# Kernel tuning notes

Measured on AMD Instinct MI355X. Metric: run time of the kernel, lower is better.

The kernel has to match this reference:

```python
import jax, jax.numpy as jnp
import numpy as np

B, M, IN, HID, A = 4096, 64, 3, 128, 64
D = 50.0                       # waveguide_bound
H_CONST = 5.0
PMAX = 10.0 ** (30 / 10 - 3)   # = 1.0 (30 dBm in Watts)
C_LIGHT = 3.0e8
FC = 6.0e9
DELTA_MIN = (C_LIGHT / FC) / 2.0  # 0.025
ALPHA = 0.2                    # LeakyReLU slope


def setup_inputs() -> dict:
    key = jax.random.key(0)
    ks = jax.random.split(key, 9)
    s = lambda k, sh: (jax.random.normal(k, sh, jnp.float32) * 0.1)
    return {
        "users": jax.random.normal(ks[0], (B, M, IN), jnp.float32),
        "W1": s(ks[1], (IN, HID)),    # GAT layer 1 projection (applied as h @ W)
        "a1": s(ks[2], (2 * HID,)),   # GAT layer 1 attention vector
        "W2": s(ks[3], (HID, HID)),   # GAT layer 2 projection
        "a2": s(ks[4], (2 * HID,)),
        "mw1": s(ks[5], (HID, 32)),   # MLP Linear(hidden, 32)
        "mb1": jnp.zeros((32,), jnp.float32),
        "mw2": s(ks[6], (32, 2 * A)), # MLP Linear(32, 2*num_antennas)
        "mb2": jnp.zeros((2 * A,), jnp.float32),
    }


def gat_layer(h, W, a):
    # Wh: [B, M, d]
    Wh = h @ W
    d = W.shape[1]
    # e[b,i,j] = leakyrelu( cat(Wh_i, Wh_j) . a ) = leakyrelu( Wh_i.a[:d] + Wh_j.a[d:] )
    si = Wh @ a[:d]          # [B, M]
    sj = Wh @ a[d:]          # [B, M]
    e = jax.nn.leaky_relu(si[:, :, None] + sj[:, None, :], ALPHA)  # [B, M, M]
    attn = jax.nn.softmax(e, axis=-1)  # softmax over neighbors j (dropout p=0 -> identity)
    h_prime = jnp.einsum('bij,bjd->bid', attn, Wh)
    return jax.nn.elu(h_prime)


def reference(users, W1, a1, W2, a2, mw1, mb1, mw2, mb2):
    h = gat_layer(users, W1, a1)
    h = gat_layer(h, W2, a2)
    pooled = jnp.max(h, axis=1)                      # [B, hidden]
    readout = jax.nn.relu(pooled @ mw1 + mb1) @ mw2 + mb2  # [B, 2A]
    raw_delta, raw_power = readout[:, :A], readout[:, A:]
    eps = 1e-6
    raw_delta = jax.nn.relu(raw_delta) + eps
    raw_power = jax.nn.relu(raw_power) + eps
    Bmax = 2.0 * D - (A - 1) * DELTA_MIN
    delta = Bmax * raw_delta / (jnp.sum(raw_delta, axis=1, keepdims=True) + eps)
    power = PMAX * raw_power / (jnp.sum(raw_power, axis=1, keepdims=True) + eps)
    return power, delta
```

## Files before the change

kernel.cpp:

```cpp
#include <hip/hip_runtime.h>

#define NBATCH 4096
#define OUT2 (NBATCH * 64)

typedef _Float16 f16;
typedef __attribute__((ext_vector_type(8))) _Float16 f16x8;
typedef __attribute__((ext_vector_type(4))) _Float16 f16x4;
typedef __attribute__((ext_vector_type(4))) float f32x4;

__device__ __forceinline__ float lrelu(float x) { return x > 0.0f ? x : 0.2f * x; }
__device__ __forceinline__ float elu1(float x)  { return x > 0.0f ? x : __expf(x) - 1.0f; }

__global__ void prep(const float* __restrict__ W2, const float* __restrict__ W1,
                     const float* __restrict__ a1, const float* __restrict__ a2,
                     f16* __restrict__ w2b, float* __restrict__ w2a, float* __restrict__ w1a) {
    const int flat = blockIdx.x * 256 + threadIdx.x;
    const int slot = flat >> 3, j = flat & 7;
    const int F2T = slot >> 8, kf = (slot >> 6) & 3, ln = slot & 63;
    const int lq = ln >> 4, lr = ln & 15;
    w2b[flat] = (f16)W2[(kf * 32 + lq * 8 + j) * 128 + F2T * 16 + lr];
    if (blockIdx.x == 0) {
        if (threadIdx.x < 128) {
            const int f1 = threadIdx.x;
            float si = 0.f, sj = 0.f;
            for (int f2 = 0; f2 < 128; ++f2) {
                const float w = W2[f1 * 128 + f2];
                si = fmaf(w, a2[f2], si);
                sj = fmaf(w, a2[128 + f2], sj);
            }
            w2a[f1] = si; w2a[128 + f1] = sj;
        } else if (threadIdx.x < 131) {
            const int c = threadIdx.x - 128;
            float si = 0.f, sj = 0.f;
            for (int f = 0; f < 128; ++f) {
                const float w = W1[c * 128 + f];
                si = fmaf(w, a1[f], si);
                sj = fmaf(w, a1[128 + f], sj);
            }
            w1a[c] = si; w1a[3 + c] = sj;
        }
    }
}

__global__ __launch_bounds__(64)
void gat_kernel(const float* __restrict__ users,
                const float* __restrict__ W1,
                const f16* __restrict__ w2b,
                const float* __restrict__ w1a,
                const float* __restrict__ w2a,
                const float* __restrict__ mw1,
                const float* __restrict__ mb1,
                const float* __restrict__ mw2,
                const float* __restrict__ mb2,
                float* __restrict__ out)
{
    const int b = blockIdx.x;
    const int lane = threadIdx.x;
    const int lr = lane & 15;
    const int lq = lane >> 4;

    __shared__ __align__(16) char smem[10752];
    f16*   sMain = (f16*)smem;
    f16*   sBn   = (f16*)(smem + 8192);
    float* sPool = (float*)(smem + 8192);
    float* sHid  = (float*)(smem + 8704);
    float* sSi   = (float*)(smem + 10240);
    float* sSj   = (float*)(smem + 10496);

    {
        const float* u = users + b * 192;
        const float x = u[lane * 3], y = u[lane * 3 + 1], z = u[lane * 3 + 2];
        sSi[lane] = fmaf(x, w1a[0], fmaf(y, w1a[1], z * w1a[2]));
        sSj[lane] = fmaf(x, w1a[3], fmaf(y, w1a[4], z * w1a[5]));
    }
    __syncthreads();
    float mj;
    {
        float v = sSj[lane];
        #pragma unroll
        for (int m = 1; m < 64; m <<= 1) v = fmaxf(v, __shfl_xor(v, m, 64));
        mj = v;
    }

    f16x8 hf[4][4];

    #pragma unroll
    for (int h = 0; h < 2; ++h) {
        f16x8 bw[4];
        #pragma unroll
        for (int ntl = 0; ntl < 4; ++ntl) {
            #pragma unroll
            for (int j = 0; j < 8; ++j) bw[ntl][j] = (f16)0.f;
            if (lq == 0) {
                #pragma unroll
                for (int j = 0; j < 3; ++j)
                    bw[ntl][j] = (f16)W1[j * 128 + h * 64 + ntl * 16 + lr];
            }
        }
        #pragma unroll
        for (int mt = 0; mt < 4; ++mt) {
            f16x8 af;
            #pragma unroll
            for (int j = 0; j < 8; ++j) af[j] = (f16)0.f;
            if (lq == 0) {
                const float* up = users + b * 192 + (mt * 16 + lr) * 3;
                af[0] = (f16)up[0]; af[1] = (f16)up[1]; af[2] = (f16)up[2];
            }
            #pragma unroll
            for (int ntl = 0; ntl < 4; ++ntl) {
                f32x4 acc = (f32x4){0.f, 0.f, 0.f, 0.f};
                acc = __builtin_amdgcn_mfma_f32_16x16x32_f16(af, bw[ntl], acc, 0, 0, 0);
                const int fl = ntl * 16 + lr;
                const int g = mt * 2 + (lq >> 1);
                const int base = fl * 64 + ((g ^ (fl & 7)) << 3) + ((lq & 1) * 4);
                f16x4 hv;
                #pragma unroll
                for (int r = 0; r < 4; ++r) hv[r] = (f16)acc[r];
                *(f16x4*)&sMain[base] = hv;
            }
        }
        __syncthreads();

        #pragma unroll
        for (int mt = 0; mt < 4; ++mt) {
            const float si = sSi[mt * 16 + lr];
            const float mi = lrelu(si + mj);
            f16x8 ap0, ap1;
            float lsum = 0.f;
            #pragma unroll
            for (int jj = 0; jj < 8; ++jj) {
                float p = __expf(lrelu(si + sSj[lq * 8 + jj]) - mi);
                f16 ph = (f16)p; lsum += (float)ph; ap0[jj] = ph;
                p = __expf(lrelu(si + sSj[32 + lq * 8 + jj]) - mi);
                ph = (f16)p; lsum += (float)ph; ap1[jj] = ph;
            }
            lsum += __shfl_xor(lsum, 16, 64);
            lsum += __shfl_xor(lsum, 32, 64);
            const float inv = 1.0f / lsum;
            float invr[4];
            #pragma unroll
            for (int r = 0; r < 4; ++r) invr[r] = __shfl(inv, lq * 4 + r, 64);

            f32x4 acc[4];
            #pragma unroll
            for (int ntl = 0; ntl < 4; ++ntl) {
                const int fl = ntl * 16 + lr;
                f16x8 b0 = *(const f16x8*)&sMain[fl * 64 + ((lq ^ (fl & 7)) << 3)];
                f16x8 b1 = *(const f16x8*)&sMain[fl * 64 + (((4 + lq) ^ (fl & 7)) << 3)];
                acc[ntl] = (f32x4){0.f, 0.f, 0.f, 0.f};
                acc[ntl] = __builtin_amdgcn_mfma_f32_16x16x32_f16(ap0, b0, acc[ntl], 0, 0, 0);
                acc[ntl] = __builtin_amdgcn_mfma_f32_16x16x32_f16(ap1, b1, acc[ntl], 0, 0, 0);
            }
            __syncthreads();
            #pragma unroll
            for (int ntl = 0; ntl < 4; ++ntl) {
                const int fl = ntl * 16 + lr;
                #pragma unroll
                for (int r = 0; r < 4; ++r) {
                    const int nl = lq * 4 + r;
                    const float v = elu1(acc[ntl][r] * invr[r]);
                    sBn[nl * 64 + (((fl >> 3) ^ (nl & 7)) << 3) + (fl & 7)] = (f16)v;
                }
            }
            __syncthreads();
            #pragma unroll
            for (int ksl = 0; ksl < 2; ++ksl)
                hf[mt][h * 2 + ksl] =
                    *(const f16x8*)&sBn[lr * 64 + (((ksl * 4 + lq) ^ (lr & 7)) << 3)];
        }
        __syncthreads();
    }

    {
        float s2i[4] = {0.f, 0.f, 0.f, 0.f}, s2j[4] = {0.f, 0.f, 0.f, 0.f};
        #pragma unroll
        for (int ks = 0; ks < 4; ++ks) {
            float wi[8], wj[8];
            *(float4*)&wi[0] = *(const float4*)&w2a[ks * 32 + lq * 8];
            *(float4*)&wi[4] = *(const float4*)&w2a[ks * 32 + lq * 8 + 4];
            *(float4*)&wj[0] = *(const float4*)&w2a[128 + ks * 32 + lq * 8];
            *(float4*)&wj[4] = *(const float4*)&w2a[128 + ks * 32 + lq * 8 + 4];
            #pragma unroll
            for (int mt = 0; mt < 4; ++mt) {
                #pragma unroll
                for (int jj = 0; jj < 8; ++jj) {
                    const float v = (float)hf[mt][ks][jj];
                    s2i[mt] = fmaf(v, wi[jj], s2i[mt]);
                    s2j[mt] = fmaf(v, wj[jj], s2j[mt]);
                }
            }
        }
        #pragma unroll
        for (int mt = 0; mt < 4; ++mt) {
            s2i[mt] += __shfl_xor(s2i[mt], 16, 64);
            s2i[mt] += __shfl_xor(s2i[mt], 32, 64);
            s2j[mt] += __shfl_xor(s2j[mt], 16, 64);
            s2j[mt] += __shfl_xor(s2j[mt], 32, 64);
        }
        if (lq == 0) {
            #pragma unroll
            for (int mt = 0; mt < 4; ++mt) {
                sSi[mt * 16 + lr] = s2i[mt];
                sSj[mt * 16 + lr] = s2j[mt];
            }
        }
        __syncthreads();
    }
    float mj2;
    {
        float v = sSj[lane];
        #pragma unroll
        for (int m = 1; m < 64; m <<= 1) v = fmaxf(v, __shfl_xor(v, m, 64));
        mj2 = v;
    }

    #pragma unroll
    for (int h = 0; h < 2; ++h) {
        #pragma unroll
        for (int f2t = 0; f2t < 4; ++f2t) {
            f16x8 bw2[4];
            #pragma unroll
            for (int kf = 0; kf < 4; ++kf)
                bw2[kf] = *(const f16x8*)(w2b + (((h * 4 + f2t) * 4 + kf) * 64 + lane) * 8);
            #pragma unroll
            for (int ntile = 0; ntile < 4; ++ntile) {
                f32x4 acc = (f32x4){0.f, 0.f, 0.f, 0.f};
                #pragma unroll
                for (int kf = 0; kf < 4; ++kf)
                    acc = __builtin_amdgcn_mfma_f32_16x16x32_f16(hf[ntile][kf], bw2[kf], acc, 0, 0, 0);
                const int fl = f2t * 16 + lr;
                const int g = ntile * 2 + (lq >> 1);
                const int base = fl * 64 + ((g ^ (fl & 7)) << 3) + ((lq & 1) * 4);
                f16x4 hv;
                #pragma unroll
                for (int r = 0; r < 4; ++r) hv[r] = (f16)acc[r];
                *(f16x4*)&sMain[base] = hv;
            }
        }
        __syncthreads();

        float mx[4] = {-1e30f, -1e30f, -1e30f, -1e30f};
        #pragma unroll
        for (int mt = 0; mt < 4; ++mt) {
            const float si = sSi[mt * 16 + lr];
            const float mi = lrelu(si + mj2);
            f16x8 ap0, ap1;
            float lsum = 0.f;
            #pragma unroll
            for (int jj = 0; jj < 8; ++jj) {
                float p = __expf(lrelu(si + sSj[lq * 8 + jj]) - mi);
                f16 ph = (f16)p; lsum += (float)ph; ap0[jj] = ph;
                p = __expf(lrelu(si + sSj[32 + lq * 8 + jj]) - mi);
                ph = (f16)p; lsum += (float)ph; ap1[jj] = ph;
            }
            lsum += __shfl_xor(lsum, 16, 64);
            lsum += __shfl_xor(lsum, 32, 64);
            const float inv = 1.0f / lsum;
            float invr[4];
            #pragma unroll
            for (int r = 0; r < 4; ++r) invr[r] = __shfl(inv, lq * 4 + r, 64);
            #pragma unroll
            for (int ntl = 0; ntl < 4; ++ntl) {
                const int fl = ntl * 16 + lr;
                f16x8 b0 = *(const f16x8*)&sMain[fl * 64 + ((lq ^ (fl & 7)) << 3)];
                f16x8 b1 = *(const f16x8*)&sMain[fl * 64 + (((4 + lq) ^ (fl & 7)) << 3)];
                f32x4 acc = (f32x4){0.f, 0.f, 0.f, 0.f};
                acc = __builtin_amdgcn_mfma_f32_16x16x32_f16(ap0, b0, acc, 0, 0, 0);
                acc = __builtin_amdgcn_mfma_f32_16x16x32_f16(ap1, b1, acc, 0, 0, 0);
                #pragma unroll
                for (int r = 0; r < 4; ++r)
                    mx[ntl] = fmaxf(mx[ntl], acc[r] * invr[r]);
            }
        }
        #pragma unroll
        for (int ntl = 0; ntl < 4; ++ntl) {
            mx[ntl] = fmaxf(mx[ntl], __shfl_xor(mx[ntl], 16, 64));
            mx[ntl] = fmaxf(mx[ntl], __shfl_xor(mx[ntl], 32, 64));
        }
        if (lq == 0) {
            #pragma unroll
            for (int ntl = 0; ntl < 4; ++ntl)
                sPool[h * 64 + ntl * 16 + lr] = elu1(mx[ntl]);
        }
        __syncthreads();
    }

    {
        const int o = lane & 31, hh = lane >> 5;
        float s = 0.f;
        #pragma unroll 8
        for (int kk = 0; kk < 64; ++kk) {
            const int c = hh * 64 + kk;
            s = fmaf(sPool[c], mw1[c * 32 + o], s);
        }
        s += __shfl_xor(s, 32, 64);
        s = fmaxf(s + mb1[o], 0.0f);
        if (lane < 32) sHid[lane] = s;
    }
    __syncthreads();
    {
        float sA = mb2[lane], sB = mb2[64 + lane];
        #pragma unroll 8
        for (int q = 0; q < 32; ++q) {
            const float hq = sHid[q];
            sA = fmaf(hq, mw2[q * 128 + lane], sA);
            sB = fmaf(hq, mw2[q * 128 + 64 + lane], sB);
        }
        const float rA = fmaxf(sA, 0.0f) + 1e-6f;
        const float rB = fmaxf(sB, 0.0f) + 1e-6f;
        float sumA = rA, sumB = rB;
        #pragma unroll
        for (int m = 1; m < 64; m <<= 1) {
            sumA += __shfl_xor(sumA, m, 64);
            sumB += __shfl_xor(sumB, m, 64);
        }
        out[b * 64 + lane]        = rB / (sumB + 1e-6f);
        out[OUT2 + b * 64 + lane] = 98.425f * rA / (sumA + 1e-6f);
    }
}

extern "C" void kernel_launch(void* const* d_in, const int* in_sizes, int n_in,
                              void* d_out, int out_size, void* d_ws, size_t ws_size,
                              hipStream_t stream) {
    const float* users = (const float*)d_in[0];
    const float* W1    = (const float*)d_in[1];
    const float* a1    = (const float*)d_in[2];
    const float* W2    = (const float*)d_in[3];
    const float* a2    = (const float*)d_in[4];
    const float* mw1   = (const float*)d_in[5];
    const float* mb1   = (const float*)d_in[6];
    const float* mw2   = (const float*)d_in[7];
    const float* mb2   = (const float*)d_in[8];
    float* out = (float*)d_out;

    f16*   w2b = (f16*)d_ws;
    float* w2a = (float*)((char*)d_ws + 32768);
    float* w1a = (float*)((char*)d_ws + 33792);

    prep<<<64, 256, 0, stream>>>(W2, W1, a1, a2, w2b, w2a, w1a);
    gat_kernel<<<NBATCH, 64, 0, stream>>>(users, W1, w2b, w1a, w2a,
                                          mw1, mb1, mw2, mb2, out);
}
```

Before: 130.6 us.

## Reassociate layer-1 GAT as (attn@users)@W1 and hoist softmax out of head loops

Layer 1 is reassociated so the attention matrix is applied to the 3-wide user features first, and the result is then projected by W1. This removes the per-head 64x64 projection staging and the transposed sBn round trip with its extra barriers. Softmax probabilities for both layers are computed once and reused across the two feature halves rather than recomputed per half. Layer 2's aggregation is reoriented so normalization and max pooling use per-node inverse sums and lane shuffles, which drops the invr broadcasts. The cost is more register pressure from holding ap/ap2 fragments, plus a slightly different fp16 rounding order.

```diff
diff --git a/kernel.cpp b/kernel.cpp
--- a/kernel.cpp
+++ b/kernel.cpp
@@ -59,13 +59,12 @@
     const int lr = lane & 15;
     const int lq = lane >> 4;
 
-    __shared__ __align__(16) char smem[10752];
+    __shared__ __align__(16) char smem[9344];
     f16*   sMain = (f16*)smem;
-    f16*   sBn   = (f16*)(smem + 8192);
-    float* sPool = (float*)(smem + 8192);
-    float* sHid  = (float*)(smem + 8704);
-    float* sSi   = (float*)(smem + 10240);
-    float* sSj   = (float*)(smem + 10496);
+    float* sSi   = (float*)(smem + 8192);
+    float* sSj   = (float*)(smem + 8448);
+    float* sPool = (float*)(smem + 8704);
+    float* sHid  = (float*)(smem + 9216);
 
     {
         const float* u = users + b * 192;
@@ -82,93 +81,89 @@
         mj = v;
     }
 
+    f16x8 ap[4][2];
+    float inv1[4];
+    #pragma unroll
+    for (int mt = 0; mt < 4; ++mt) {
+        const float si = sSi[mt * 16 + lr];
+        const float mi = lrelu(si + mj);
+        float lsum = 0.f;
+        #pragma unroll
+        for (int jj = 0; jj < 8; ++jj) {
+            float p = __expf(lrelu(si + sSj[lq * 8 + jj]) - mi);
+            f16 ph = (f16)p; lsum += (float)ph; ap[mt][0][jj] = ph;
+            p = __expf(lrelu(si + sSj[32 + lq * 8 + jj]) - mi);
+            ph = (f16)p; lsum += (float)ph; ap[mt][1][jj] = ph;
+        }
+        lsum += __shfl_xor(lsum, 16, 64);
+        lsum += __shfl_xor(lsum, 32, 64);
+        inv1[mt] = 1.0f / lsum;
+    }
+
+    f16x8 af2[2];
+    #pragma unroll
+    for (int ks = 0; ks < 2; ++ks) {
+        #pragma unroll
+        for (int jj = 0; jj < 8; ++jj) {
+            const int node = ks * 32 + lq * 8 + jj;
+            af2[ks][jj] = (lr < 3) ? (f16)users[b * 192 + node * 3 + lr] : (f16)0.f;
+        }
+    }
+    f32x4 d1[4];
+    #pragma unroll
+    for (int nt = 0; nt < 4; ++nt) {
+        d1[nt] = (f32x4){0.f, 0.f, 0.f, 0.f};
+        d1[nt] = __builtin_amdgcn_mfma_f32_16x16x32_f16(af2[0], ap[nt][0], d1[nt], 0, 0, 0);
+        d1[nt] = __builtin_amdgcn_mfma_f32_16x16x32_f16(af2[1], ap[nt][1], d1[nt], 0, 0, 0);
+    }
+    f16x8 bfr[4];
+    #pragma unroll
+    for (int nt = 0; nt < 4; ++nt) {
+        const float c0 = __shfl(d1[nt][0], lr, 64);
+        const float c1 = __shfl(d1[nt][1], lr, 64);
+        const float c2 = __shfl(d1[nt][2], lr, 64);
+        #pragma unroll
+        for (int jj = 0; jj < 8; ++jj) bfr[nt][jj] = (f16)0.f;
+        if (lq == 0) {
+            bfr[nt][0] = (f16)c0; bfr[nt][1] = (f16)c1; bfr[nt][2] = (f16)c2;
+        }
+    }
+
     f16x8 hf[4][4];
-
     #pragma unroll
     for (int h = 0; h < 2; ++h) {
-        f16x8 bw[4];
-        #pragma unroll
-        for (int ntl = 0; ntl < 4; ++ntl) {
-            #pragma unroll
-            for (int j = 0; j < 8; ++j) bw[ntl][j] = (f16)0.f;
+        __syncthreads();
+        #pragma unroll
+        for (int ftl = 0; ftl < 4; ++ftl) {
+            f16x8 af3;
+            #pragma unroll
+            for (int jj = 0; jj < 8; ++jj) af3[jj] = (f16)0.f;
             if (lq == 0) {
                 #pragma unroll
-                for (int j = 0; j < 3; ++j)
-                    bw[ntl][j] = (f16)W1[j * 128 + h * 64 + ntl * 16 + lr];
-            }
-        }
-        #pragma unroll
-        for (int mt = 0; mt < 4; ++mt) {
-            f16x8 af;
-            #pragma unroll
-            for (int j = 0; j < 8; ++j) af[j] = (f16)0.f;
-            if (lq == 0) {
-                const float* up = users + b * 192 + (mt * 16 + lr) * 3;
-                af[0] = (f16)up[0]; af[1] = (f16)up[1]; af[2] = (f16)up[2];
-            }
-            #pragma unroll
-            for (int ntl = 0; ntl < 4; ++ntl) {
+                for (int jj = 0; jj < 3; ++jj)
+                    af3[jj] = (f16)W1[jj * 128 + (h * 4 + ftl) * 16 + lr];
+            }
+            #pragma unroll
+            for (int nt = 0; nt < 4; ++nt) {
                 f32x4 acc = (f32x4){0.f, 0.f, 0.f, 0.f};
-                acc = __builtin_amdgcn_mfma_f32_16x16x32_f16(af, bw[ntl], acc, 0, 0, 0);
-                const int fl = ntl * 16 + lr;
-                const int g = mt * 2 + (lq >> 1);
-                const int base = fl * 64 + ((g ^ (fl & 7)) << 3) + ((lq & 1) * 4);
+                acc = __builtin_amdgcn_mfma_f32_16x16x32_f16(af3, bfr[nt], acc, 0, 0, 0);
                 f16x4 hv;
                 #pragma unroll
-                for (int r = 0; r < 4; ++r) hv[r] = (f16)acc[r];
-                *(f16x4*)&sMain[base] = hv;
-            }
-        }
-        __syncthreads();
-
-        #pragma unroll
-        for (int mt = 0; mt < 4; ++mt) {
-            const float si = sSi[mt * 16 + lr];
-            const float mi = lrelu(si + mj);
-            f16x8 ap0, ap1;
-            float lsum = 0.f;
-            #pragma unroll
-            for (int jj = 0; jj < 8; ++jj) {
-                float p = __expf(lrelu(si + sSj[lq * 8 + jj]) - mi);
-                f16 ph = (f16)p; lsum += (float)ph; ap0[jj] = ph;
-                p = __expf(lrelu(si + sSj[32 + lq * 8 + jj]) - mi);
-                ph = (f16)p; lsum += (float)ph; ap1[jj] = ph;
-            }
-            lsum += __shfl_xor(lsum, 16, 64);
-            lsum += __shfl_xor(lsum, 32, 64);
-            const float inv = 1.0f / lsum;
-            float invr[4];
-            #pragma unroll
-            for (int r = 0; r < 4; ++r) invr[r] = __shfl(inv, lq * 4 + r, 64);
-
-            f32x4 acc[4];
-            #pragma unroll
-            for (int ntl = 0; ntl < 4; ++ntl) {
-                const int fl = ntl * 16 + lr;
-                f16x8 b0 = *(const f16x8*)&sMain[fl * 64 + ((lq ^ (fl & 7)) << 3)];
-                f16x8 b1 = *(const f16x8*)&sMain[fl * 64 + (((4 + lq) ^ (fl & 7)) << 3)];
-                acc[ntl] = (f32x4){0.f, 0.f, 0.f, 0.f};
-                acc[ntl] = __builtin_amdgcn_mfma_f32_16x16x32_f16(ap0, b0, acc[ntl], 0, 0, 0);
-                acc[ntl] = __builtin_amdgcn_mfma_f32_16x16x32_f16(ap1, b1, acc[ntl], 0, 0, 0);
-            }
-            __syncthreads();
-            #pragma unroll
-            for (int ntl = 0; ntl < 4; ++ntl) {
-                const int fl = ntl * 16 + lr;
-                #pragma unroll
-                for (int r = 0; r < 4; ++r) {
-                    const int nl = lq * 4 + r;
-                    const float v = elu1(acc[ntl][r] * invr[r]);
-                    sBn[nl * 64 + (((fl >> 3) ^ (nl & 7)) << 3) + (fl & 7)] = (f16)v;
-                }
-            }
-            __syncthreads();
+                for (int r = 0; r < 4; ++r) hv[r] = (f16)elu1(acc[r] * inv1[nt]);
+                const int n = nt * 16 + lr;
+                const int g = 2 * ftl + (lq >> 1);
+                *(f16x4*)&sMain[n * 64 + ((g ^ (n & 7)) << 3) + ((lq & 1) * 4)] = hv;
+            }
+        }
+        __syncthreads();
+        #pragma unroll
+        for (int nt = 0; nt < 4; ++nt) {
+            const int n = nt * 16 + lr;
             #pragma unroll
             for (int ksl = 0; ksl < 2; ++ksl)
-                hf[mt][h * 2 + ksl] =
-                    *(const f16x8*)&sBn[lr * 64 + (((ksl * 4 + lq) ^ (lr & 7)) << 3)];
-        }
-        __syncthreads();
+                hf[nt][h * 2 + ksl] =
+                    *(const f16x8*)&sMain[n * 64 + (((ksl * 4 + lq) ^ (n & 7)) << 3)];
+        }
     }
 
     {
@@ -214,8 +209,28 @@
         mj2 = v;
     }
 
+    f16x8 ap2[4][2];
+    float inv2[4];
+    #pragma unroll
+    for (int mt = 0; mt < 4; ++mt) {
+        const float si = sSi[mt * 16 + lr];
+        const float mi = lrelu(si + mj2);
+        float lsum = 0.f;
+        #pragma unroll
+        for (int jj = 0; jj < 8; ++jj) {
+            float p = __expf(lrelu(si + sSj[lq * 8 + jj]) - mi);
+            f16 ph = (f16)p; lsum += (float)ph; ap2[mt][0][jj] = ph;
+            p = __expf(lrelu(si + sSj[32 + lq * 8 + jj]) - mi);
+            ph = (f16)p; lsum += (float)ph; ap2[mt][1][jj] = ph;
+        }
+        lsum += __shfl_xor(lsum, 16, 64);
+        lsum += __shfl_xor(lsum, 32, 64);
+        inv2[mt] = 1.0f / lsum;
+    }
+
     #pragma unroll
     for (int h = 0; h < 2; ++h) {
+        __syncthreads();
         #pragma unroll
         for (int f2t = 0; f2t < 4; ++f2t) {
             f16x8 bw2[4];
@@ -230,57 +245,41 @@
                     acc = __builtin_amdgcn_mfma_f32_16x16x32_f16(hf[ntile][kf], bw2[kf], acc, 0, 0, 0);
                 const int fl = f2t * 16 + lr;
                 const int g = ntile * 2 + (lq >> 1);
-                const int base = fl * 64 + ((g ^ (fl & 7)) << 3) + ((lq & 1) * 4);
                 f16x4 hv;
                 #pragma unroll
                 for (int r = 0; r < 4; ++r) hv[r] = (f16)acc[r];
-                *(f16x4*)&sMain[base] = hv;
-            }
-        }
-        __syncthreads();
-
-        float mx[4] = {-1e30f, -1e30f, -1e30f, -1e30f};
-        #pragma unroll
-        for (int mt = 0; mt < 4; ++mt) {
-            const float si = sSi[mt * 16 + lr];
-            const float mi = lrelu(si + mj2);
-            f16x8 ap0, ap1;
-            float lsum = 0.f;
-            #pragma unroll
-            for (int jj = 0; jj < 8; ++jj) {
-                float p = __expf(lrelu(si + sSj[lq * 8 + jj]) - mi);
-                f16 ph = (f16)p; lsum += (float)ph; ap0[jj] = ph;
-                p = __expf(lrelu(si + sSj[32 + lq * 8 + jj]) - mi);
-                ph = (f16)p; lsum += (float)ph; ap1[jj] = ph;
-            }
-            lsum += __shfl_xor(lsum, 16, 64);
-            lsum += __shfl_xor(lsum, 32, 64);
-            const float inv = 1.0f / lsum;
-            float invr[4];
-            #pragma unroll
-            for (int r = 0; r < 4; ++r) invr[r] = __shfl(inv, lq * 4 + r, 64);
-            #pragma unroll
-            for (int ntl = 0; ntl < 4; ++ntl) {
-                const int fl = ntl * 16 + lr;
-                f16x8 b0 = *(const f16x8*)&sMain[fl * 64 + ((lq ^ (fl & 7)) << 3)];
-                f16x8 b1 = *(const f16x8*)&sMain[fl * 64 + (((4 + lq) ^ (fl & 7)) << 3)];
+                *(f16x4*)&sMain[fl * 64 + ((g ^ (fl & 7)) << 3) + ((lq & 1) * 4)] = hv;
+            }
+        }
+        __syncthreads();
+
+        #pragma unroll
+        for (int ftl = 0; ftl < 4; ++ftl) {
+            const int fl = ftl * 16 + lr;
+            f16x8 b0 = *(const f16x8*)&sMain[fl * 64 + ((lq ^ (fl & 7)) << 3)];
+            f16x8 b1 = *(const f16x8*)&sMain[fl * 64 + (((4 + lq) ^ (fl & 7)) << 3)];
+            f32x4 mx4 = (f32x4){-1e30f, -1e30f, -1e30f, -1e30f};
+            #pragma unroll
+            for (int mt = 0; mt < 4; ++mt) {
                 f32x4 acc = (f32x4){0.f, 0.f, 0.f, 0.f};
-                acc = __builtin_amdgcn_mfma_f32_16x16x32_f16(ap0, b0, acc, 0, 0, 0);
-                acc = __builtin_amdgcn_mfma_f32_16x16x32_f16(ap1, b1, acc, 0, 0, 0);
+                acc = __builtin_amdgcn_mfma_f32_16x16x32_f16(b0, ap2[mt][0], acc, 0, 0, 0);
+                acc = __builtin_amdgcn_mfma_f32_16x16x32_f16(b1, ap2[mt][1], acc, 0, 0, 0);
                 #pragma unroll
                 for (int r = 0; r < 4; ++r)
-                    mx[ntl] = fmaxf(mx[ntl], acc[r] * invr[r]);
-            }
-        }
-        #pragma unroll
-        for (int ntl = 0; ntl < 4; ++ntl) {
-            mx[ntl] = fmaxf(mx[ntl], __shfl_xor(mx[ntl], 16, 64));
-            mx[ntl] = fmaxf(mx[ntl], __shfl_xor(mx[ntl], 32, 64));
-        }
-        if (lq == 0) {
-            #pragma unroll
-            for (int ntl = 0; ntl < 4; ++ntl)
-                sPool[h * 64 + ntl * 16 + lr] = elu1(mx[ntl]);
+                    mx4[r] = fmaxf(mx4[r], acc[r] * inv2[mt]);
+            }
+            #pragma unroll
+            for (int m = 1; m < 16; m <<= 1) {
+                #pragma unroll
+                for (int r = 0; r < 4; ++r)
+                    mx4[r] = fmaxf(mx4[r], __shfl_xor(mx4[r], m, 64));
+            }
+            if (lr == 0) {
+                float4 pv;
+                pv.x = elu1(mx4[0]); pv.y = elu1(mx4[1]);
+                pv.z = elu1(mx4[2]); pv.w = elu1(mx4[3]);
+                *(float4*)&sPool[h * 64 + ftl * 16 + lq * 4] = pv;
+            }
         }
         __syncthreads();
     }
```

Result: faster. 121.5 us (-7.0%).
